# Kernel tuning notes

Hardware: AMD Instinct MI355X
Metric: run time of the kernel (lower is better)

The kernel has to match this reference:

```python
import jax, jax.numpy as jnp
import numpy as np

N_NODES = 100000


def gcn_conv(x, edge_index, W, b):
    # GCNConv with add_self_loops=True, normalize=True (symmetric norm):
    # out = D^{-1/2} (A + I) D^{-1/2} (x @ W) + b
    n = x.shape[0]
    h = x @ W  # transform first (PyG applies lin before propagate)
    src, dst = edge_index[0], edge_index[1]
    ones = jnp.ones(src.shape[0], dtype=h.dtype)
    # degree with self-loops: in-degree + 1
    deg = jax.ops.segment_sum(ones, dst, num_segments=n) + 1.0
    dinv = jax.lax.rsqrt(deg)  # deg >= 1, always finite
    # per-edge normalized messages, scatter-add to dst
    msg = h[src] * (dinv[src] * dinv[dst])[:, None]
    agg = jax.ops.segment_sum(msg, dst, num_segments=n)
    # self-loop contribution: norm = dinv[i]^2
    agg = agg + h * (dinv * dinv)[:, None]
    return agg + b


def setup_inputs() -> dict:
    key = jax.random.key(0)
    ks = jax.random.split(key, 8)
    x = jax.random.normal(ks[0], (N_NODES, 256), dtype=jnp.float32)
    edge_index = jax.random.randint(ks[1], (2, 3200000), 0, N_NODES, dtype=jnp.int32)
    W1 = jax.random.normal(ks[2], (256, 32), dtype=jnp.float32) * (1.0 / np.sqrt(256))
    b1 = jnp.zeros((32,), dtype=jnp.float32)
    Wm = jax.random.normal(ks[3], (32, 16), dtype=jnp.float32) * (1.0 / np.sqrt(32))
    bm = jnp.zeros((16,), dtype=jnp.float32)
    Wv = jax.random.normal(ks[4], (32, 16), dtype=jnp.float32) * (1.0 / np.sqrt(32))
    bv = jnp.zeros((16,), dtype=jnp.float32)
    return {"x": x, "edge_index": edge_index, "W1": W1, "b1": b1,
            "Wm": Wm, "bm": bm, "Wv": Wv, "bv": bv}


def reference(x, edge_index, W1, b1, Wm, bm, Wv, bv):
    h = jax.nn.relu(gcn_conv(x, edge_index, W1, b1))
    mu = gcn_conv(h, edge_index, Wm, bm)
    sigma = gcn_conv(h, edge_index, Wv, bv)
    return (mu, sigma)
```

## Files before the change

kernel.cpp:

```cpp
#include <hip/hip_runtime.h>
#include <hip/hip_fp16.h>

#define NNODES 100000
#define NEDGES 3200000
#define F_IN   256
#define F_HID  32
#define F_OUT  16

#define NB   196
#define NPB  512
#define CAP  20480
#define NCHUNK 256
#define CHUNK  12500

#define GRID1 ((NNODES + 63) / 64)
#define XT_RS 130

typedef _Float16 half_t;
typedef half_t half8 __attribute__((ext_vector_type(8)));
typedef float f32x4 __attribute__((ext_vector_type(4)));
typedef const __attribute__((address_space(1))) unsigned int* gas_u32;
typedef __attribute__((address_space(3))) unsigned int* las_u32;


__global__ void k_init(int* __restrict__ bcur) {
    if (threadIdx.x < NB) bcur[threadIdx.x] = threadIdx.x * CAP;
}

__global__ __launch_bounds__(256) void k_phaseA(
        const int* __restrict__ src, const int* __restrict__ dst,
        int* __restrict__ bcur, unsigned int* __restrict__ rec) {
    __shared__ int lh[NB];
    __shared__ int lcur[NB];
    int t = threadIdx.x;
    int e0 = blockIdx.x * CHUNK;
    for (int i = t; i < NB; i += 256) lh[i] = 0;
    __syncthreads();
    for (int i = t; i < CHUNK; i += 256)
        atomicAdd(&lh[dst[e0 + i] >> 9], 1);
    __syncthreads();
    for (int i = t; i < NB; i += 256)
        lcur[i] = lh[i] ? atomicAdd(&bcur[i], lh[i]) : 0;
    __syncthreads();
    for (int i = t; i < CHUNK; i += 256) {
        int s = src[e0 + i], d = dst[e0 + i];
        int b = d >> 9;
        int pos = atomicAdd(&lcur[b], 1);
        rec[pos] = ((unsigned)s << 9) | (unsigned)(d & 511);
    }
}

__global__ __launch_bounds__(512) void k_phaseB(
        const unsigned int* __restrict__ rec, const int* __restrict__ bcur,
        int* __restrict__ rowptr, int* __restrict__ cnt,
        float* __restrict__ dinv, int* __restrict__ csr) {
    __shared__ int lh[NPB];
    __shared__ int lsc[NPB];
    __shared__ int wsum[8];
    int t = threadIdx.x, b = blockIdx.x;
    int lo = b * CAP, hi = bcur[b];
    lh[t] = 0;
    __syncthreads();
    for (int i = lo + t; i < hi; i += 512)
        atomicAdd(&lh[rec[i] & 511], 1);
    __syncthreads();
    int lane = t & 63, w = t >> 6;
    int my = lh[t];
    int v = my;
    #pragma unroll
    for (int d = 1; d < 64; d <<= 1) {
        int tmp = __shfl_up(v, d, 64);
        if (lane >= d) v += tmp;
    }
    if (lane == 63) wsum[w] = v;
    __syncthreads();
    if (w == 0) {
        int s = (lane < 8) ? wsum[lane] : 0;
        #pragma unroll
        for (int d = 1; d < 8; d <<= 1) {
            int tmp = __shfl_up(s, d, 64);
            if (lane >= d) s += tmp;
        }
        if (lane < 8) wsum[lane] = s;
    }
    __syncthreads();
    int ex = v + (w > 0 ? wsum[w - 1] : 0) - my;
    lsc[t] = ex;
    int node = b * NPB + t;
    if (node < NNODES) {
        rowptr[node] = lo + ex;
        cnt[node] = my;
        dinv[node] = rsqrtf((float)my + 1.0f);
    }
    __syncthreads();
    for (int i = lo + t; i < hi; i += 512) {
        unsigned r = rec[i];
        int dl = r & 511;
        int p = atomicAdd(&lsc[dl], 1);
        csr[lo + p] = (int)(r >> 9);
    }
}


__global__ __launch_bounds__(256) void k_gemm1(
        const float* __restrict__ x, const float* __restrict__ W1,
        const float* __restrict__ dinv, __half2* __restrict__ g1) {
    __shared__ half_t Wt[32 * 264];
    __shared__ float xt[4][16 * XT_RS];
    int t = threadIdx.x;
    int wave = t >> 6, lane = t & 63;
    int m = lane & 15, q = lane >> 4;
    int row0 = blockIdx.x * 64 + wave * 16;

    for (int i = t; i < F_IN * F_HID; i += 256) {
        int k = i >> 5, f = i & 31;
        Wt[f * 264 + k] = (half_t)W1[i];
    }
    __syncthreads();

    half8 B[2][8];
    #pragma unroll
    for (int ft = 0; ft < 2; ++ft)
        #pragma unroll
        for (int kc = 0; kc < 8; ++kc)
            B[ft][kc] = *(const half8*)&Wt[(ft * 16 + m) * 264 + kc * 32 + q * 8];

    float* xw = xt[wave];
    f32x4 acc0 = {0.f, 0.f, 0.f, 0.f};
    f32x4 acc1 = {0.f, 0.f, 0.f, 0.f};
    #pragma unroll
    for (int kh = 0; kh < 2; ++kh) {
        #pragma unroll
        for (int r = 0; r < 16; ++r) {
            int grow = row0 + r; if (grow >= NNODES) grow = NNODES - 1;
            const float* gp = &x[(size_t)grow * F_IN + kh * 128 + lane];
            __builtin_amdgcn_global_load_lds((gas_u32)gp,
                (las_u32)&xw[r * XT_RS], 4, 0, 0);
            __builtin_amdgcn_global_load_lds((gas_u32)(gp + 64),
                (las_u32)&xw[r * XT_RS + 64], 4, 0, 0);
        }
        asm volatile("s_waitcnt vmcnt(0)" ::: "memory");
        #pragma unroll
        for (int kc = 0; kc < 4; ++kc) {
            const float* sp = &xw[m * XT_RS + kc * 32 + q * 8];
            float2 x0 = *(const float2*)sp;
            float2 x1 = *(const float2*)(sp + 2);
            float2 x2 = *(const float2*)(sp + 4);
            float2 x3 = *(const float2*)(sp + 6);
            half8 A;
            A[0] = (half_t)x0.x; A[1] = (half_t)x0.y;
            A[2] = (half_t)x1.x; A[3] = (half_t)x1.y;
            A[4] = (half_t)x2.x; A[5] = (half_t)x2.y;
            A[6] = (half_t)x3.x; A[7] = (half_t)x3.y;
            acc0 = __builtin_amdgcn_mfma_f32_16x16x32_f16(A, B[0][kh * 4 + kc], acc0, 0, 0, 0);
            acc1 = __builtin_amdgcn_mfma_f32_16x16x32_f16(A, B[1][kh * 4 + kc], acc1, 0, 0, 0);
        }
        if (kh == 0) asm volatile("s_waitcnt lgkmcnt(0)" ::: "memory");
    }

    __syncthreads();
    float* sb = xw;
    #pragma unroll
    for (int r = 0; r < 4; ++r) {
        int rl = q * 4 + r;
        int grow = row0 + rl; if (grow >= NNODES) grow = NNODES - 1;
        float dv = dinv[grow];
        sb[rl * 33 + m]      = acc0[r] * dv;
        sb[rl * 33 + 16 + m] = acc1[r] * dv;
    }
    __syncthreads();
    int rl = (t >> 2) & 15;
    int w2 = t >> 6;
    int c0 = (t & 3) * 8;
    int grow = blockIdx.x * 64 + w2 * 16 + rl;
    if (grow < NNODES) {
        const float* sp = &xt[w2][rl * 33 + c0];
        __half2 h0 = __floats2half2_rn(sp[0], sp[1]);
        __half2 h1 = __floats2half2_rn(sp[2], sp[3]);
        __half2 h2 = __floats2half2_rn(sp[4], sp[5]);
        __half2 h3 = __floats2half2_rn(sp[6], sp[7]);
        __half2* gp = &g1[(size_t)grow * 16 + (c0 >> 1)];
        gp[0] = h0; gp[1] = h1; gp[2] = h2; gp[3] = h3;
    }
}


__global__ __launch_bounds__(256) void k_gather_l1(
        const int* __restrict__ rowptr, const int* __restrict__ cnt,
        const int* __restrict__ csr,
        const float* __restrict__ dinv, const __half2* __restrict__ g,
        const float* __restrict__ b1, const float* __restrict__ Wm,
        const float* __restrict__ Wv, __half2* __restrict__ g2) {
    __shared__ float Wcat[F_HID * 32];
    __shared__ float hrow[16][F_HID + 2];
    int tx = threadIdx.x;
    for (int idx = tx; idx < F_HID * 32; idx += 256) {
        int k = idx >> 5, j = idx & 31;
        Wcat[idx] = (j < F_OUT) ? Wm[k * F_OUT + j] : Wv[k * F_OUT + (j - F_OUT)];
    }
    int f2 = tx & 15;
    int lr = tx >> 4;
    int node = blockIdx.x * 16 + lr;
    int start = rowptr[node], end = start + cnt[node];
    float2 acc = __half22float2(g[(size_t)node * 16 + f2]);
    int j = start;
    for (; j + 4 <= end; j += 4) {
        int s0 = csr[j], s1 = csr[j + 1], s2 = csr[j + 2], s3 = csr[j + 3];
        float2 a0 = __half22float2(g[(size_t)s0 * 16 + f2]);
        float2 a1 = __half22float2(g[(size_t)s1 * 16 + f2]);
        float2 a2 = __half22float2(g[(size_t)s2 * 16 + f2]);
        float2 a3 = __half22float2(g[(size_t)s3 * 16 + f2]);
        acc.x += (a0.x + a1.x) + (a2.x + a3.x);
        acc.y += (a0.y + a1.y) + (a2.y + a3.y);
    }
    for (; j < end; ++j) {
        float2 a = __half22float2(g[(size_t)csr[j] * 16 + f2]);
        acc.x += a.x; acc.y += a.y;
    }
    float dv = dinv[node];
    float h0 = dv * acc.x + b1[2 * f2];
    float h1 = dv * acc.y + b1[2 * f2 + 1];
    hrow[lr][2 * f2]     = h0 > 0.f ? h0 : 0.f;
    hrow[lr][2 * f2 + 1] = h1 > 0.f ? h1 : 0.f;
    __syncthreads();
    float o0 = 0.f, o1 = 0.f;
    #pragma unroll
    for (int k = 0; k < F_HID; ++k) {
        float hv = hrow[lr][k];
        o0 = fmaf(hv, Wcat[k * 32 + 2 * f2], o0);
        o1 = fmaf(hv, Wcat[k * 32 + 2 * f2 + 1], o1);
    }
    g2[(size_t)node * 16 + f2] = __floats2half2_rn(o0 * dv, o1 * dv);
}


__global__ __launch_bounds__(256) void k_gather_out(
        const int* __restrict__ rowptr, const int* __restrict__ cnt,
        const int* __restrict__ csr,
        const float* __restrict__ dinv, const __half2* __restrict__ g,
        const float* __restrict__ bm, const float* __restrict__ bv,
        float* __restrict__ out) {
    int tx = threadIdx.x;
    int f2 = tx & 15;
    int node = blockIdx.x * 16 + (tx >> 4);
    int start = rowptr[node], end = start + cnt[node];
    float2 acc = __half22float2(g[(size_t)node * 16 + f2]);
    int j = start;
    for (; j + 4 <= end; j += 4) {
        int s0 = csr[j], s1 = csr[j + 1], s2 = csr[j + 2], s3 = csr[j + 3];
        float2 a0 = __half22float2(g[(size_t)s0 * 16 + f2]);
        float2 a1 = __half22float2(g[(size_t)s1 * 16 + f2]);
        float2 a2 = __half22float2(g[(size_t)s2 * 16 + f2]);
        float2 a3 = __half22float2(g[(size_t)s3 * 16 + f2]);
        acc.x += (a0.x + a1.x) + (a2.x + a3.x);
        acc.y += (a0.y + a1.y) + (a2.y + a3.y);
    }
    for (; j < end; ++j) {
        float2 a = __half22float2(g[(size_t)csr[j] * 16 + f2]);
        acc.x += a.x; acc.y += a.y;
    }
    float dv = dinv[node];
    int f = 2 * f2;
    if (f < F_OUT) {
        float2 o = { dv * acc.x + bm[f], dv * acc.y + bm[f + 1] };
        *(float2*)&out[(size_t)node * F_OUT + f] = o;
    } else {
        float2 o = { dv * acc.x + bv[f - F_OUT], dv * acc.y + bv[f - F_OUT + 1] };
        *(float2*)&out[(size_t)NNODES * F_OUT + (size_t)node * F_OUT + (f - F_OUT)] = o;
    }
}


extern "C" void kernel_launch(void* const* d_in, const int* in_sizes, int n_in,
                              void* d_out, int out_size, void* d_ws, size_t ws_size,
                              hipStream_t stream) {
    const float* x   = (const float*)d_in[0];
    const int*   ei  = (const int*)  d_in[1];
    const float* W1  = (const float*)d_in[2];
    const float* b1  = (const float*)d_in[3];
    const float* Wm  = (const float*)d_in[4];
    const float* bm  = (const float*)d_in[5];
    const float* Wv  = (const float*)d_in[6];
    const float* bv  = (const float*)d_in[7];
    float* out = (float*)d_out;

    const int* src = ei;
    const int* dst = ei + NEDGES;

    char* ws = (char*)d_ws;
    float*        dinv   = (float*)ws;        ws += 100352 * 4;
    int*          bcur   = (int*)ws;          ws += 256 * 4;
    int*          rowptr = (int*)ws;          ws += 100352 * 4;
    int*          cnt    = (int*)ws;          ws += 100352 * 4;
    int*          csr    = (int*)ws;          ws += (size_t)NB * CAP * 4;
    unsigned int* rec    = (unsigned int*)ws; ws += (size_t)NB * CAP * 4;
    __half2*      g2     = (__half2*)ws;

    __half2* g1 = (__half2*)rec;

    k_init  <<<1, 256, 0, stream>>>(bcur);
    k_phaseA<<<NCHUNK, 256, 0, stream>>>(src, dst, bcur, rec);
    k_phaseB<<<NB, 512, 0, stream>>>(rec, bcur, rowptr, cnt, dinv, csr);

    k_gemm1<<<GRID1, 256, 0, stream>>>(x, W1, dinv, g1);

    k_gather_l1<<<NNODES / 16, 256, 0, stream>>>(rowptr, cnt, csr, dinv, g1, b1, Wm, Wv, g2);

    k_gather_out<<<NNODES / 16, 256, 0, stream>>>(rowptr, cnt, csr, dinv, g2, bm, bv, out);
}
```

Measured before the change: 361.6 us.

## Replace two-level bucketed CSR build with global atomic degree count and scan

Replaces the bucketed two-pass CSR construction, which used local histograms, bucket records and per-bucket scatter, with a direct global-atomic degree count. A three-kernel prefix scan follows, then a global-atomic placement of each edge's source into CSR. This removes the intermediate record buffer and its extra read/write pass, and packs CSR tightly. In exchange it issues many more global atomics, on contended per-node counters with random addressing, and adds more kernel launches.

```diff
diff --git a/kernel.cpp b/kernel.cpp
--- a/kernel.cpp
+++ b/kernel.cpp
@@ -7,11 +7,9 @@
 #define F_HID  32
 #define F_OUT  16
 
-#define NB   196
-#define NPB  512
-#define CAP  20480
-#define NCHUNK 256
-#define CHUNK  12500
+#define NND_AL 100352
+#define NSCAN  392
+#define EGRID  2048
 
 #define GRID1 ((NNODES + 63) / 64)
 #define XT_RS 130
@@ -23,49 +21,25 @@
 typedef __attribute__((address_space(3))) unsigned int* las_u32;
 
 
-__global__ void k_init(int* __restrict__ bcur) {
-    if (threadIdx.x < NB) bcur[threadIdx.x] = threadIdx.x * CAP;
-}
-
-__global__ __launch_bounds__(256) void k_phaseA(
-        const int* __restrict__ src, const int* __restrict__ dst,
-        int* __restrict__ bcur, unsigned int* __restrict__ rec) {
-    __shared__ int lh[NB];
-    __shared__ int lcur[NB];
-    int t = threadIdx.x;
-    int e0 = blockIdx.x * CHUNK;
-    for (int i = t; i < NB; i += 256) lh[i] = 0;
-    __syncthreads();
-    for (int i = t; i < CHUNK; i += 256)
-        atomicAdd(&lh[dst[e0 + i] >> 9], 1);
-    __syncthreads();
-    for (int i = t; i < NB; i += 256)
-        lcur[i] = lh[i] ? atomicAdd(&bcur[i], lh[i]) : 0;
-    __syncthreads();
-    for (int i = t; i < CHUNK; i += 256) {
-        int s = src[e0 + i], d = dst[e0 + i];
-        int b = d >> 9;
-        int pos = atomicAdd(&lcur[b], 1);
-        rec[pos] = ((unsigned)s << 9) | (unsigned)(d & 511);
-    }
-}
-
-__global__ __launch_bounds__(512) void k_phaseB(
-        const unsigned int* __restrict__ rec, const int* __restrict__ bcur,
-        int* __restrict__ rowptr, int* __restrict__ cnt,
-        float* __restrict__ dinv, int* __restrict__ csr) {
-    __shared__ int lh[NPB];
-    __shared__ int lsc[NPB];
-    __shared__ int wsum[8];
+__global__ __launch_bounds__(256) void k_zero(int* __restrict__ deg) {
+    deg[blockIdx.x * 256 + threadIdx.x] = 0;
+}
+
+__global__ __launch_bounds__(256) void k_deg(
+        const int* __restrict__ dst, int* __restrict__ deg) {
+    int stride = gridDim.x * 256;
+    for (int i = blockIdx.x * 256 + threadIdx.x; i < NEDGES; i += stride)
+        atomicAdd(&deg[dst[i]], 1);
+}
+
+__global__ __launch_bounds__(256) void k_scan1(
+        const int* __restrict__ deg, int* __restrict__ rowptr,
+        int* __restrict__ partial) {
+    __shared__ int wsum[4];
     int t = threadIdx.x, b = blockIdx.x;
-    int lo = b * CAP, hi = bcur[b];
-    lh[t] = 0;
-    __syncthreads();
-    for (int i = lo + t; i < hi; i += 512)
-        atomicAdd(&lh[rec[i] & 511], 1);
-    __syncthreads();
+    int node = b * 256 + t;
+    int my = (node < NNODES) ? deg[node] : 0;
     int lane = t & 63, w = t >> 6;
-    int my = lh[t];
     int v = my;
     #pragma unroll
     for (int d = 1; d < 64; d <<= 1) {
@@ -74,30 +48,59 @@
     }
     if (lane == 63) wsum[w] = v;
     __syncthreads();
-    if (w == 0) {
-        int s = (lane < 8) ? wsum[lane] : 0;
-        #pragma unroll
-        for (int d = 1; d < 8; d <<= 1) {
-            int tmp = __shfl_up(s, d, 64);
-            if (lane >= d) s += tmp;
-        }
-        if (lane < 8) wsum[lane] = s;
-    }
-    __syncthreads();
-    int ex = v + (w > 0 ? wsum[w - 1] : 0) - my;
-    lsc[t] = ex;
-    int node = b * NPB + t;
+    if (t == 0) {
+        int s = 0;
+        #pragma unroll
+        for (int i = 0; i < 4; ++i) { int x = wsum[i]; wsum[i] = s; s += x; }
+        partial[b] = s;
+    }
+    __syncthreads();
+    rowptr[node] = v - my + wsum[w];
+}
+
+__global__ __launch_bounds__(512) void k_scan2(int* __restrict__ partial) {
+    __shared__ int wsum[8];
+    int t = threadIdx.x;
+    int my = (t < NSCAN) ? partial[t] : 0;
+    int lane = t & 63, w = t >> 6;
+    int v = my;
+    #pragma unroll
+    for (int d = 1; d < 64; d <<= 1) {
+        int tmp = __shfl_up(v, d, 64);
+        if (lane >= d) v += tmp;
+    }
+    if (lane == 63) wsum[w] = v;
+    __syncthreads();
+    if (t == 0) {
+        int s = 0;
+        #pragma unroll
+        for (int i = 0; i < 8; ++i) { int x = wsum[i]; wsum[i] = s; s += x; }
+    }
+    __syncthreads();
+    if (t < NSCAN) partial[t] = v - my + wsum[w];
+}
+
+__global__ __launch_bounds__(256) void k_scan3(
+        const int* __restrict__ deg, int* __restrict__ rowptr,
+        int* __restrict__ cur, float* __restrict__ dinv,
+        const int* __restrict__ partial) {
+    int node = blockIdx.x * 256 + threadIdx.x;
     if (node < NNODES) {
-        rowptr[node] = lo + ex;
-        cnt[node] = my;
-        dinv[node] = rsqrtf((float)my + 1.0f);
-    }
-    __syncthreads();
-    for (int i = lo + t; i < hi; i += 512) {
-        unsigned r = rec[i];
-        int dl = r & 511;
-        int p = atomicAdd(&lsc[dl], 1);
-        csr[lo + p] = (int)(r >> 9);
+        int rp = rowptr[node] + partial[blockIdx.x];
+        rowptr[node] = rp;
+        cur[node] = rp;
+        dinv[node] = rsqrtf((float)deg[node] + 1.0f);
+    }
+}
+
+__global__ __launch_bounds__(256) void k_place(
+        const int* __restrict__ src, const int* __restrict__ dst,
+        int* __restrict__ cur, int* __restrict__ csr) {
+    int stride = gridDim.x * 256;
+    for (int i = blockIdx.x * 256 + threadIdx.x; i < NEDGES; i += stride) {
+        int d = dst[i];
+        int pos = atomicAdd(&cur[d], 1);
+        csr[pos] = src[i];
     }
 }
 
@@ -288,23 +291,25 @@
     const int* dst = ei + NEDGES;
 
     char* ws = (char*)d_ws;
-    float*        dinv   = (float*)ws;        ws += 100352 * 4;
-    int*          bcur   = (int*)ws;          ws += 256 * 4;
-    int*          rowptr = (int*)ws;          ws += 100352 * 4;
-    int*          cnt    = (int*)ws;          ws += 100352 * 4;
-    int*          csr    = (int*)ws;          ws += (size_t)NB * CAP * 4;
-    unsigned int* rec    = (unsigned int*)ws; ws += (size_t)NB * CAP * 4;
-    __half2*      g2     = (__half2*)ws;
-
-    __half2* g1 = (__half2*)rec;
-
-    k_init  <<<1, 256, 0, stream>>>(bcur);
-    k_phaseA<<<NCHUNK, 256, 0, stream>>>(src, dst, bcur, rec);
-    k_phaseB<<<NB, 512, 0, stream>>>(rec, bcur, rowptr, cnt, dinv, csr);
+    float*   dinv    = (float*)ws;   ws += NND_AL * 4;
+    int*     rowptr  = (int*)ws;     ws += NND_AL * 4;
+    int*     deg     = (int*)ws;     ws += NND_AL * 4;
+    int*     cur     = (int*)ws;     ws += NND_AL * 4;
+    int*     partial = (int*)ws;     ws += 512 * 4;
+    int*     csr     = (int*)ws;     ws += (size_t)NEDGES * 4;
+    __half2* g1      = (__half2*)ws; ws += (size_t)NNODES * 16 * 4;
+    __half2* g2      = (__half2*)ws;
+
+    k_zero <<<NSCAN, 256, 0, stream>>>(deg);
+    k_deg  <<<EGRID, 256, 0, stream>>>(dst, deg);
+    k_scan1<<<NSCAN, 256, 0, stream>>>(deg, rowptr, partial);
+    k_scan2<<<1, 512, 0, stream>>>(partial);
+    k_scan3<<<NSCAN, 256, 0, stream>>>(deg, rowptr, cur, dinv, partial);
+    k_place<<<EGRID, 256, 0, stream>>>(src, dst, cur, csr);
 
     k_gemm1<<<GRID1, 256, 0, stream>>>(x, W1, dinv, g1);
 
-    k_gather_l1<<<NNODES / 16, 256, 0, stream>>>(rowptr, cnt, csr, dinv, g1, b1, Wm, Wv, g2);
-
-    k_gather_out<<<NNODES / 16, 256, 0, stream>>>(rowptr, cnt, csr, dinv, g2, bm, bv, out);
-}
+    k_gather_l1<<<NNODES / 16, 256, 0, stream>>>(rowptr, deg, csr, dinv, g1, b1, Wm, Wv, g2);
+
+    k_gather_out<<<NNODES / 16, 256, 0, stream>>>(rowptr, deg, csr, dinv, g2, bm, bv, out);
+}
```

After: 675.9 us. +86.9%, slower.
